# Kernel optimization log

Measured on AMD Instinct MI355X. Metric: run time of the kernel, lower is better.

Reference implementation:

```python
import jax, jax.numpy as jnp
import numpy as np

D_MODEL = 1024
NUM_HEADS = 16
D_K = D_MODEL // NUM_HEADS


def setup_inputs() -> dict:
    key = jax.random.key(0)
    ks = jax.random.split(key, 11)
    B, S = 2, 2048
    scale = 1.0 / np.sqrt(D_MODEL)
    inp = {
        "Q": jax.random.normal(ks[0], (B, S, D_MODEL), jnp.float32),
        "K": jax.random.normal(ks[1], (B, S, D_MODEL), jnp.float32),
        "V": jax.random.normal(ks[2], (B, S, D_MODEL), jnp.float32),
        # per-head projection weights stacked on head axis: [H, d_model, d_k]
        "Wq": jax.random.uniform(ks[3], (NUM_HEADS, D_MODEL, D_K), jnp.float32, -scale, scale),
        "bq": jax.random.uniform(ks[4], (NUM_HEADS, D_K), jnp.float32, -scale, scale),
        "Wk": jax.random.uniform(ks[5], (NUM_HEADS, D_MODEL, D_K), jnp.float32, -scale, scale),
        "bk": jax.random.uniform(ks[6], (NUM_HEADS, D_K), jnp.float32, -scale, scale),
        "Wv": jax.random.uniform(ks[7], (NUM_HEADS, D_MODEL, D_K), jnp.float32, -scale, scale),
        "bv": jax.random.uniform(ks[8], (NUM_HEADS, D_K), jnp.float32, -scale, scale),
        "Wo": jax.random.uniform(ks[9], (D_MODEL, D_MODEL), jnp.float32, -scale, scale),
        "bo": jax.random.uniform(ks[10], (D_MODEL,), jnp.float32, -scale, scale),
    }
    return inp


def reference(Q, K, V, Wq, bq, Wk, bk, Wv, bv, Wo, bo):
    # Batched equivalent of the per-head loop: project all heads at once.
    q = jnp.einsum("bsd,hdk->bhsk", Q, Wq) + bq[None, :, None, :]
    k = jnp.einsum("bsd,hdk->bhsk", K, Wk) + bk[None, :, None, :]
    v = jnp.einsum("bsd,hdk->bhsk", V, Wv) + bv[None, :, None, :]
    scores = jnp.einsum("bhqk,bhmk->bhqm", q, k) / jnp.sqrt(jnp.float32(D_K))
    weights = jax.nn.softmax(scores, axis=-1)
    attn = jnp.einsum("bhqm,bhmk->bhqk", weights, v)  # [B,H,S,d_k]
    B, H, S, Dk = attn.shape
    concat = attn.transpose(0, 2, 1, 3).reshape(B, S, H * Dk)  # head-order concat
    return concat @ Wo.T + bo
```

## Files before the change

### kernel.cpp

```cpp
#include <hip/hip_runtime.h>
#include <math.h>

#define BATCH 2
#define SLEN 2048
#define DM 1024
#define NH 16
#define DK 64
#define STILES (SLEN / 64)

typedef __attribute__((ext_vector_type(8))) __bf16 bf16x8;
typedef __attribute__((ext_vector_type(4))) float f32x4;

__device__ __forceinline__ unsigned short f2bf(float x) {
  unsigned u = __builtin_bit_cast(unsigned, x);
  unsigned r = (u + 0x7fffu + ((u >> 16) & 1u)) >> 16;
  return (unsigned short)r;
}
__device__ __forceinline__ float bf2f(unsigned short b) {
  unsigned u = ((unsigned)b) << 16;
  return __builtin_bit_cast(float, u);
}
__device__ __forceinline__ void splitbf(float x, unsigned short& h,
                                        unsigned short& l) {
  unsigned u = __builtin_bit_cast(unsigned, x);
  h = (unsigned short)(u >> 16);
  float hf = __builtin_bit_cast(float, u & 0xffff0000u);
  l = (unsigned short)(__builtin_bit_cast(unsigned, x - hf) >> 16);
}

__device__ __forceinline__ void gld16(const unsigned short* g,
                                      unsigned short* l) {
  __builtin_amdgcn_global_load_lds(
      (const __attribute__((address_space(1))) void*)g,
      (__attribute__((address_space(3))) void*)l, 16, 0, 0);
}

__global__ __launch_bounds__(256)
void convert_w(const float* __restrict__ Wq, const float* __restrict__ Wk,
               const float* __restrict__ Wv, unsigned short* __restrict__ Wqt,
               unsigned short* __restrict__ Wkt,
               unsigned short* __restrict__ Wvt) {
  const int kb = blockIdx.x, h = blockIdx.y, z = blockIdx.z;
  const float* W = (z == 0 ? Wq : z == 1 ? Wk : Wv) +
                   ((size_t)h * DM + kb * 64) * DK;
  unsigned short* D = (z == 0 ? Wqt : z == 1 ? Wkt : Wvt);

  __shared__ float T[64][65];
  const int tid = threadIdx.x;
  {
    int r = tid >> 2, c0 = (tid & 3) * 16;
#pragma unroll
    for (int i = 0; i < 4; ++i) {
      float4 f = *(const float4*)(W + (size_t)r * DK + c0 + i * 4);
      T[r][c0 + i * 4 + 0] = f.x;
      T[r][c0 + i * 4 + 1] = f.y;
      T[r][c0 + i * 4 + 2] = f.z;
      T[r][c0 + i * 4 + 3] = f.w;
    }
  }
  __syncthreads();
  int j = tid >> 2, p = tid & 3;
  int n = h * 64 + j;
  int kloc = p * 16;
  unsigned short hi[16], lo[16];
#pragma unroll
  for (int i = 0; i < 16; ++i) splitbf(T[kloc + i][j], hi[i], lo[i]);
  int kglob = kb * 64 + kloc;
  int blk = kglob >> 5;
  int c0 = (kglob & 31) >> 3;
  int key = n & 7;
  unsigned short* rowp = D + (size_t)n * 2048 + blk * 64;
  uint4 u0, u1;
  u0.x = (unsigned)hi[0] | ((unsigned)hi[1] << 16);
  u0.y = (unsigned)hi[2] | ((unsigned)hi[3] << 16);
  u0.z = (unsigned)hi[4] | ((unsigned)hi[5] << 16);
  u0.w = (unsigned)hi[6] | ((unsigned)hi[7] << 16);
  u1.x = (unsigned)hi[8] | ((unsigned)hi[9] << 16);
  u1.y = (unsigned)hi[10] | ((unsigned)hi[11] << 16);
  u1.z = (unsigned)hi[12] | ((unsigned)hi[13] << 16);
  u1.w = (unsigned)hi[14] | ((unsigned)hi[15] << 16);
  *(uint4*)(rowp + ((c0 ^ key)) * 8) = u0;
  *(uint4*)(rowp + (((c0 + 1) ^ key)) * 8) = u1;
  u0.x = (unsigned)lo[0] | ((unsigned)lo[1] << 16);
  u0.y = (unsigned)lo[2] | ((unsigned)lo[3] << 16);
  u0.z = (unsigned)lo[4] | ((unsigned)lo[5] << 16);
  u0.w = (unsigned)lo[6] | ((unsigned)lo[7] << 16);
  u1.x = (unsigned)lo[8] | ((unsigned)lo[9] << 16);
  u1.y = (unsigned)lo[10] | ((unsigned)lo[11] << 16);
  u1.z = (unsigned)lo[12] | ((unsigned)lo[13] << 16);
  u1.w = (unsigned)lo[14] | ((unsigned)lo[15] << 16);
  *(uint4*)(rowp + (((c0 + 4) ^ key)) * 8) = u0;
  *(uint4*)(rowp + (((c0 + 5) ^ key)) * 8) = u1;
}

__global__ __launch_bounds__(256)
void convert_wo(const float* __restrict__ Wo, unsigned short* __restrict__ Wot) {
  const int n = blockIdx.x;
  const int t = threadIdx.x;
  const int k0 = t * 4;
  float4 f = *(const float4*)(Wo + (size_t)n * DM + k0);
  ushort4 h4, l4;
  splitbf(f.x, h4.x, l4.x);
  splitbf(f.y, h4.y, l4.y);
  splitbf(f.z, h4.z, l4.z);
  splitbf(f.w, h4.w, l4.w);
  int blk = k0 >> 5, ch = (k0 & 31) >> 3, off = k0 & 7, key = n & 7;
  unsigned short* rowp = Wot + (size_t)n * 2048 + blk * 64;
  *(ushort4*)(rowp + ((ch ^ key)) * 8 + off) = h4;
  *(ushort4*)(rowp + (((ch + 4) ^ key)) * 8 + off) = l4;
}

__global__ __launch_bounds__(256)
void proj_gemm(const float* __restrict__ Qin, const float* __restrict__ Kin,
               const float* __restrict__ Vin,
               const unsigned short* __restrict__ Wqt,
               const unsigned short* __restrict__ Wkt,
               const unsigned short* __restrict__ Wvt,
               const float* __restrict__ bq, const float* __restrict__ bk,
               const float* __restrict__ bv, unsigned short* __restrict__ q_all,
               unsigned short* __restrict__ k_all,
               unsigned short* __restrict__ vt) {
  const int ntile = blockIdx.x, mt = blockIdx.y, z = blockIdx.z;
  const float* A = (z == 0 ? Qin : z == 1 ? Kin : Vin);
  const unsigned short* B = (z == 0 ? Wqt : z == 1 ? Wkt : Wvt);
  const float* bias = (z == 0 ? bq : z == 1 ? bk : bv);

  __shared__ alignas(16) unsigned short As[2][128 * 64];
  __shared__ alignas(16) unsigned short Bs[2][128 * 64];

  const int tid = threadIdx.x;
  const int lane = tid & 63, w = tid >> 6;
  const int l15 = lane & 15, quad = lane >> 4;
  const int wm = (w & 1) * 64, wn = (w >> 1) * 64;
  const int kx = l15 & 7;

  const float* Ap = A + (size_t)(mt * 128) * DM;
  const unsigned short* Bp = B + (size_t)(ntile * 128) * 2048;

  float4 areg[4];
#pragma unroll
  for (int it = 0; it < 4; ++it) {
    int c = tid + it * 256;
    int r = c >> 3, seg = c & 7;
    areg[it] = *(const float4*)(Ap + (size_t)r * DM + seg * 4);
  }
#pragma unroll
  for (int it = 0; it < 4; ++it) {
    int s = tid + it * 256;
    int r = s >> 3, seg = s & 7;
    gld16(Bp + (size_t)r * 2048 + seg * 8, &Bs[0][s * 8]);
  }

  f32x4 acc[4][4];
#pragma unroll
  for (int i = 0; i < 4; ++i)
#pragma unroll
    for (int j = 0; j < 4; ++j) acc[i][j] = (f32x4){0.f, 0.f, 0.f, 0.f};

  int cur = 0;
  for (int kk = 0; kk < 32; ++kk) {
#pragma unroll
    for (int it = 0; it < 4; ++it) {
      int c = tid + it * 256;
      int r = c >> 3, seg = c & 7;
      int key = r & 7, ch = seg >> 1, off = (seg & 1) * 4;
      ushort4 h4, l4;
      splitbf(areg[it].x, h4.x, l4.x);
      splitbf(areg[it].y, h4.y, l4.y);
      splitbf(areg[it].z, h4.z, l4.z);
      splitbf(areg[it].w, h4.w, l4.w);
      *(ushort4*)&As[cur][r * 64 + ((ch ^ key)) * 8 + off] = h4;
      *(ushort4*)&As[cur][r * 64 + (((ch + 4) ^ key)) * 8 + off] = l4;
    }
    __syncthreads();

    if (kk + 1 < 32) {
      int k0n = (kk + 1) * 32;
#pragma unroll
      for (int it = 0; it < 4; ++it) {
        int c = tid + it * 256;
        int r = c >> 3, seg = c & 7;
        areg[it] = *(const float4*)(Ap + (size_t)r * DM + k0n + seg * 4);
      }
#pragma unroll
      for (int it = 0; it < 4; ++it) {
        int s = tid + it * 256;
        int r = s >> 3, seg = s & 7;
        gld16(Bp + (size_t)r * 2048 + (k0n >> 5) * 64 + seg * 8,
              &Bs[cur ^ 1][s * 8]);
      }
    }

    bf16x8 ah[4], al[4];
#pragma unroll
    for (int i = 0; i < 4; ++i) {
      const unsigned short* p = &As[cur][(wm + i * 16 + l15) * 64];
      ah[i] = *(const bf16x8*)(p + ((quad ^ kx)) * 8);
      al[i] = *(const bf16x8*)(p + (((quad + 4) ^ kx)) * 8);
    }
#pragma unroll
    for (int j = 0; j < 4; ++j) {
      const unsigned short* p = &Bs[cur][(wn + j * 16 + l15) * 64];
      bf16x8 bh = *(const bf16x8*)(p + ((quad ^ kx)) * 8);
      bf16x8 bl = *(const bf16x8*)(p + (((quad + 4) ^ kx)) * 8);
#pragma unroll
      for (int i = 0; i < 4; ++i) {
        acc[i][j] = __builtin_amdgcn_mfma_f32_16x16x32_bf16(ah[i], bh, acc[i][j], 0, 0, 0);
        acc[i][j] = __builtin_amdgcn_mfma_f32_16x16x32_bf16(al[i], bh, acc[i][j], 0, 0, 0);
        acc[i][j] = __builtin_amdgcn_mfma_f32_16x16x32_bf16(ah[i], bl, acc[i][j], 0, 0, 0);
      }
    }
    cur ^= 1;
  }

  if (z <= 1) {
    unsigned short* dst = (z == 0 ? q_all : k_all);
#pragma unroll
    for (int i = 0; i < 4; ++i)
#pragma unroll
      for (int j = 0; j < 4; ++j) {
        int n = ntile * 128 + wn + j * 16 + l15;
        int hh_ = n >> 6, d = n & 63;
        int chi = (d >> 5) * 8 + ((d & 31) >> 3);
        float bn = bias[n];
#pragma unroll
        for (int r = 0; r < 4; ++r) {
          int m = mt * 128 + wm + i * 16 + quad * 4 + r;
          int key = m & 15;
          size_t rb = (size_t)m * 2048 + hh_ * 128;
          unsigned short hv, lv;
          splitbf(acc[i][j][r] + bn, hv, lv);
          dst[rb + ((chi ^ key)) * 8 + (d & 7)] = hv;
          dst[rb + (((chi + 4) ^ key)) * 8 + (d & 7)] = lv;
        }
      }
  } else {
#pragma unroll
    for (int i = 0; i < 4; ++i)
#pragma unroll
      for (int j = 0; j < 4; ++j) {
        int n = ntile * 128 + wn + j * 16 + l15;
        int h = n >> 6, d = n & 63;
        float bn = bias[n];
        int m0 = mt * 128 + wm + i * 16 + quad * 4;
        int b = m0 >> 11, s0_ = m0 & 2047;
        int kt = s0_ >> 6, sl = s0_ & 63;
        int ch = sl >> 3, off = sl & 7, key = d & 15;
        ushort4 h4, l4;
        splitbf(acc[i][j][0] + bn, h4.x, l4.x);
        splitbf(acc[i][j][1] + bn, h4.y, l4.y);
        splitbf(acc[i][j][2] + bn, h4.z, l4.z);
        splitbf(acc[i][j][3] + bn, h4.w, l4.w);
        size_t base =
            (size_t)(b * NH + h) * 262144 + (size_t)d * 4096 + kt * 128;
        *(ushort4*)(vt + base + ((ch ^ key)) * 8 + off) = h4;
        *(ushort4*)(vt + base + (((ch + 8) ^ key)) * 8 + off) = l4;
      }
  }
}

__global__ __launch_bounds__(256)
void out_gemm(const unsigned short* __restrict__ a_all,
              const unsigned short* __restrict__ Wot,
              const float* __restrict__ bo, float* __restrict__ out) {
  const int ntile = blockIdx.x, mt = blockIdx.y;

  __shared__ alignas(16) unsigned short As[2][64 * 64];
  __shared__ alignas(16) unsigned short Bs[2][128 * 64];

  const int tid = threadIdx.x;
  const int lane = tid & 63, w = tid >> 6;
  const int l15 = lane & 15, quad = lane >> 4;
  const int wn = w * 32;
  const int kx = l15 & 7;

  const unsigned short* Ap = a_all + (size_t)(mt * 64) * 2048;
  const unsigned short* Bp = Wot + (size_t)(ntile * 128) * 2048;

#pragma unroll
  for (int it = 0; it < 2; ++it) {
    int s = tid + it * 256;
    int r = s >> 3, seg = s & 7;
    gld16(Ap + (size_t)r * 2048 + seg * 8, &As[0][s * 8]);
  }
#pragma unroll
  for (int it = 0; it < 4; ++it) {
    int s = tid + it * 256;
    int r = s >> 3, seg = s & 7;
    gld16(Bp + (size_t)r * 2048 + seg * 8, &Bs[0][s * 8]);
  }

  f32x4 acc[4][2];
#pragma unroll
  for (int i = 0; i < 4; ++i)
#pragma unroll
    for (int j = 0; j < 2; ++j) acc[i][j] = (f32x4){0.f, 0.f, 0.f, 0.f};

  int cur = 0;
  for (int kk = 0; kk < 32; ++kk) {
    __syncthreads();

    if (kk + 1 < 32) {
      int blk = ((kk + 1)) * 64;
#pragma unroll
      for (int it = 0; it < 2; ++it) {
        int s = tid + it * 256;
        int r = s >> 3, seg = s & 7;
        gld16(Ap + (size_t)r * 2048 + blk + seg * 8, &As[cur ^ 1][s * 8]);
      }
#pragma unroll
      for (int it = 0; it < 4; ++it) {
        int s = tid + it * 256;
        int r = s >> 3, seg = s & 7;
        gld16(Bp + (size_t)r * 2048 + blk + seg * 8, &Bs[cur ^ 1][s * 8]);
      }
    }

    bf16x8 ah[4], al[4];
#pragma unroll
    for (int i = 0; i < 4; ++i) {
      const unsigned short* p = &As[cur][(i * 16 + l15) * 64];
      ah[i] = *(const bf16x8*)(p + ((quad ^ kx)) * 8);
      al[i] = *(const bf16x8*)(p + (((quad + 4) ^ kx)) * 8);
    }
#pragma unroll
    for (int j = 0; j < 2; ++j) {
      const unsigned short* p = &Bs[cur][(wn + j * 16 + l15) * 64];
      bf16x8 bh = *(const bf16x8*)(p + ((quad ^ kx)) * 8);
      bf16x8 bl = *(const bf16x8*)(p + (((quad + 4) ^ kx)) * 8);
#pragma unroll
      for (int i = 0; i < 4; ++i) {
        acc[i][j] = __builtin_amdgcn_mfma_f32_16x16x32_bf16(ah[i], bh, acc[i][j], 0, 0, 0);
        acc[i][j] = __builtin_amdgcn_mfma_f32_16x16x32_bf16(al[i], bh, acc[i][j], 0, 0, 0);
        acc[i][j] = __builtin_amdgcn_mfma_f32_16x16x32_bf16(ah[i], bl, acc[i][j], 0, 0, 0);
      }
    }
    cur ^= 1;
  }

#pragma unroll
  for (int i = 0; i < 4; ++i)
#pragma unroll
    for (int j = 0; j < 2; ++j) {
      int n = ntile * 128 + wn + j * 16 + l15;
      float bn = bo[n];
#pragma unroll
      for (int r = 0; r < 4; ++r) {
        int m = mt * 64 + i * 16 + quad * 4 + r;
        out[(size_t)m * DM + n] = acc[i][j][r] + bn;
      }
    }
}

__global__ __launch_bounds__(256)
void attn_kernel(const unsigned short* __restrict__ q_all,
                 const unsigned short* __restrict__ k_all,
                 const unsigned short* __restrict__ vt,
                 unsigned short* __restrict__ a_all) {
  const int qt = blockIdx.x, h = blockIdx.y, b = blockIdx.z;
  const unsigned short* vp = vt + (size_t)(b * NH + h) * 262144;

  __shared__ alignas(16) unsigned short Ks[64 * 128];
  __shared__ alignas(16) unsigned short Vs[64 * 128];
  __shared__ alignas(16) unsigned short Ps[128 * 64];

  const int tid = threadIdx.x;
  const int lane = tid & 63;
  const int w = tid >> 6;
  const int l15 = lane & 15;
  const int quad = lane >> 4;

  bf16x8 qf[2][2][2];
#pragma unroll
  for (int rt = 0; rt < 2; ++rt) {
    const unsigned short* qrow =
        q_all + (size_t)(b * SLEN + qt * 128 + w * 32 + rt * 16 + l15) * 2048 +
        h * 128;
#pragma unroll
    for (int kb = 0; kb < 2; ++kb) {
      qf[rt][kb][0] = *(const bf16x8*)(qrow + ((kb * 8 + quad) ^ l15) * 8);
      qf[rt][kb][1] = *(const bf16x8*)(qrow + ((kb * 8 + quad + 4) ^ l15) * 8);
    }
  }

  f32x4 o[2][4];
  float lpart[2][4];
#pragma unroll
  for (int rt = 0; rt < 2; ++rt)
#pragma unroll
    for (int nt = 0; nt < 4; ++nt) {
      o[rt][nt] = (f32x4){0.f, 0.f, 0.f, 0.f};
      lpart[rt][nt] = 0.f;
    }

  for (int kt = 0; kt < STILES; ++kt) {
    const unsigned short* ksrc =
        k_all + (size_t)(b * SLEN + kt * 64) * 2048 + h * 128;
#pragma unroll
    for (int it = 0; it < 4; ++it) {
      int ss = it * 256 + tid;
      int r = ss >> 4, p = ss & 15;
      gld16(ksrc + (size_t)r * 2048 + p * 8, &Ks[ss * 8]);
    }
#pragma unroll
    for (int it = 0; it < 4; ++it) {
      int ss = it * 256 + tid;
      int d = ss >> 4, p = ss & 15;
      gld16(vp + (size_t)d * 4096 + kt * 128 + p * 8, &Vs[ss * 8]);
    }
    __syncthreads();

    f32x4 sc[2][4];
#pragma unroll
    for (int rt = 0; rt < 2; ++rt)
#pragma unroll
      for (int ct = 0; ct < 4; ++ct) sc[rt][ct] = (f32x4){0.f, 0.f, 0.f, 0.f};
#pragma unroll
    for (int ct = 0; ct < 4; ++ct) {
      const unsigned short* kbase = &Ks[(ct * 16 + l15) * 128];
#pragma unroll
      for (int kb = 0; kb < 2; ++kb) {
        bf16x8 kh = *(const bf16x8*)(kbase + ((kb * 8 + quad) ^ l15) * 8);
        bf16x8 kl = *(const bf16x8*)(kbase + ((kb * 8 + quad + 4) ^ l15) * 8);
#pragma unroll
        for (int rt = 0; rt < 2; ++rt) {
          sc[rt][ct] = __builtin_amdgcn_mfma_f32_16x16x32_bf16(qf[rt][kb][0], kh, sc[rt][ct], 0, 0, 0);
          sc[rt][ct] = __builtin_amdgcn_mfma_f32_16x16x32_bf16(qf[rt][kb][0], kl, sc[rt][ct], 0, 0, 0);
          sc[rt][ct] = __builtin_amdgcn_mfma_f32_16x16x32_bf16(qf[rt][kb][1], kh, sc[rt][ct], 0, 0, 0);
        }
      }
    }

#pragma unroll
    for (int rt = 0; rt < 2; ++rt)
#pragma unroll
      for (int ct = 0; ct < 4; ++ct)
#pragma unroll
        for (int r = 0; r < 4; ++r) {
          float e = __expf(sc[rt][ct][r] * 0.125f);
          lpart[rt][r] += e;
          int prow = w * 32 + rt * 16 + quad * 4 + r;
          int pkey = (prow >> 1) & 7;
          Ps[prow * 64 + (((ct * 2 + (l15 >> 3)) ^ pkey)) * 8 + (l15 & 7)] =
              f2bf(e);
        }
    __syncthreads();

    int rk = (l15 >> 1) & 7;
#pragma unroll
    for (int kb = 0; kb < 2; ++kb) {
      bf16x8 pf[2];
#pragma unroll
      for (int rt = 0; rt < 2; ++rt)
        pf[rt] = *(const bf16x8*)(&Ps[(w * 32 + rt * 16 + l15) * 64 +
                                      (((kb * 4 + quad) ^ rk)) * 8]);
#pragma unroll
      for (int nt = 0; nt < 4; ++nt) {
        const unsigned short* vb = &Vs[(nt * 16 + l15) * 128];
        bf16x8 vh = *(const bf16x8*)(vb + (((kb * 4 + quad) ^ l15)) * 8);
        bf16x8 vl = *(const bf16x8*)(vb + (((kb * 4 + quad + 8) ^ l15)) * 8);
#pragma unroll
        for (int rt = 0; rt < 2; ++rt) {
          o[rt][nt] = __builtin_amdgcn_mfma_f32_16x16x32_bf16(pf[rt], vh, o[rt][nt], 0, 0, 0);
          o[rt][nt] = __builtin_amdgcn_mfma_f32_16x16x32_bf16(pf[rt], vl, o[rt][nt], 0, 0, 0);
        }
      }
    }
    __syncthreads();
  }

#pragma unroll
  for (int rt = 0; rt < 2; ++rt) {
    float inv[4];
#pragma unroll
    for (int r = 0; r < 4; ++r) {
      float lv = lpart[rt][r];
#pragma unroll
      for (int m = 1; m < 16; m <<= 1) lv += __shfl_xor(lv, m, 64);
      inv[r] = 1.f / lv;
    }
#pragma unroll
    for (int nt = 0; nt < 4; ++nt) {
      int c = h * 64 + nt * 16 + l15;
      int Bb = c >> 5;
      int d32 = c & 31;
      int ch = d32 >> 3, off = d32 & 7;
#pragma unroll
      for (int r = 0; r < 4; ++r) {
        float val = o[rt][nt][r] * inv[r];
        int srow = qt * 128 + w * 32 + rt * 16 + quad * 4 + r;
        int key = srow & 7;
        size_t g = (size_t)(b * SLEN + srow) * 2048 + Bb * 64;
        unsigned short hv, lv2;
        splitbf(val, hv, lv2);
        a_all[g + ((ch ^ key)) * 8 + off] = hv;
        a_all[g + (((ch + 4) ^ key)) * 8 + off] = lv2;
      }
    }
  }
}

extern "C" void kernel_launch(void* const* d_in, const int* in_sizes, int n_in,
                              void* d_out, int out_size, void* d_ws,
                              size_t ws_size, hipStream_t stream) {
  (void)in_sizes; (void)n_in; (void)out_size; (void)ws_size;
  const float* Q = (const float*)d_in[0];
  const float* K = (const float*)d_in[1];
  const float* V = (const float*)d_in[2];
  const float* Wq = (const float*)d_in[3];
  const float* bq = (const float*)d_in[4];
  const float* Wk = (const float*)d_in[5];
  const float* bk = (const float*)d_in[6];
  const float* Wv = (const float*)d_in[7];
  const float* bv = (const float*)d_in[8];
  const float* Wo = (const float*)d_in[9];
  const float* bo = (const float*)d_in[10];
  float* out = (float*)d_out;

  unsigned short* us = (unsigned short*)d_ws;
  const size_t M8 = 8u * 1024 * 1024;
  unsigned short* q_all = us;
  unsigned short* k_all = us + M8;
  unsigned short* vt = us + 2 * M8;
  unsigned short* a_all = us + 3 * M8;
  unsigned short* Wqt = a_all;
  unsigned short* Wkt = a_all + 2 * 1024 * 1024;
  unsigned short* Wvt = a_all + 4 * 1024 * 1024;
  unsigned short* Wot = q_all;

  convert_w<<<dim3(16, 16, 3), 256, 0, stream>>>(Wq, Wk, Wv, Wqt, Wkt, Wvt);
  proj_gemm<<<dim3(8, 32, 3), 256, 0, stream>>>(Q, K, V, Wqt, Wkt, Wvt, bq,
                                                bk, bv, q_all, k_all, vt);
  attn_kernel<<<dim3(SLEN / 128, NH, BATCH), 256, 0, stream>>>(q_all, k_all,
                                                               vt, a_all);
  convert_wo<<<dim3(1024), 256, 0, stream>>>(Wo, Wot);
  out_gemm<<<dim3(8, 64), 256, 0, stream>>>(a_all, Wot, bo, out);
}
```

Measured before the change: 371.1 us.

## Pre-split activations to bf16 hi/lo and double-buffer K/V tiles in attention

```diff
diff --git a/kernel.cpp b/kernel.cpp
--- a/kernel.cpp
+++ b/kernel.cpp
@@ -15,10 +15,6 @@
   unsigned u = __builtin_bit_cast(unsigned, x);
   unsigned r = (u + 0x7fffu + ((u >> 16) & 1u)) >> 16;
   return (unsigned short)r;
-}
-__device__ __forceinline__ float bf2f(unsigned short b) {
-  unsigned u = ((unsigned)b) << 16;
-  return __builtin_bit_cast(float, u);
 }
 __device__ __forceinline__ void splitbf(float x, unsigned short& h,
                                         unsigned short& l) {
@@ -94,6 +90,26 @@
 }
 
 __global__ __launch_bounds__(256)
+void convert_x(const float* __restrict__ Q, const float* __restrict__ K,
+               const float* __restrict__ V, unsigned short* __restrict__ Xp) {
+  const int m = blockIdx.x, z = blockIdx.y;
+  const float* src = (z == 0 ? Q : z == 1 ? K : V) + (size_t)m * DM;
+  unsigned short* dst =
+      Xp + (size_t)z * (8u * 1024 * 1024) + (size_t)m * 2048;
+  const int k0 = threadIdx.x * 4;
+  float4 f = *(const float4*)(src + k0);
+  ushort4 h4, l4;
+  splitbf(f.x, h4.x, l4.x);
+  splitbf(f.y, h4.y, l4.y);
+  splitbf(f.z, h4.z, l4.z);
+  splitbf(f.w, h4.w, l4.w);
+  int blk = k0 >> 5, ch = (k0 & 31) >> 3, off = k0 & 7, key = m & 7;
+  unsigned short* rowp = dst + blk * 64;
+  *(ushort4*)(rowp + ((ch ^ key)) * 8 + off) = h4;
+  *(ushort4*)(rowp + (((ch + 4) ^ key)) * 8 + off) = l4;
+}
+
+__global__ __launch_bounds__(256)
 void convert_wo(const float* __restrict__ Wo, unsigned short* __restrict__ Wot) {
   const int n = blockIdx.x;
   const int t = threadIdx.x;
@@ -111,8 +127,7 @@
 }
 
 __global__ __launch_bounds__(256)
-void proj_gemm(const float* __restrict__ Qin, const float* __restrict__ Kin,
-               const float* __restrict__ Vin,
+void proj_gemm(const unsigned short* __restrict__ Xp,
                const unsigned short* __restrict__ Wqt,
                const unsigned short* __restrict__ Wkt,
                const unsigned short* __restrict__ Wvt,
@@ -121,7 +136,6 @@
                unsigned short* __restrict__ k_all,
                unsigned short* __restrict__ vt) {
   const int ntile = blockIdx.x, mt = blockIdx.y, z = blockIdx.z;
-  const float* A = (z == 0 ? Qin : z == 1 ? Kin : Vin);
   const unsigned short* B = (z == 0 ? Wqt : z == 1 ? Wkt : Wvt);
   const float* bias = (z == 0 ? bq : z == 1 ? bk : bv);
 
@@ -134,20 +148,15 @@
   const int wm = (w & 1) * 64, wn = (w >> 1) * 64;
   const int kx = l15 & 7;
 
-  const float* Ap = A + (size_t)(mt * 128) * DM;
+  const unsigned short* Ap =
+      Xp + (size_t)z * (8u * 1024 * 1024) + (size_t)(mt * 128) * 2048;
   const unsigned short* Bp = B + (size_t)(ntile * 128) * 2048;
 
-  float4 areg[4];
-#pragma unroll
-  for (int it = 0; it < 4; ++it) {
-    int c = tid + it * 256;
-    int r = c >> 3, seg = c & 7;
-    areg[it] = *(const float4*)(Ap + (size_t)r * DM + seg * 4);
-  }
 #pragma unroll
   for (int it = 0; it < 4; ++it) {
     int s = tid + it * 256;
     int r = s >> 3, seg = s & 7;
+    gld16(Ap + (size_t)r * 2048 + seg * 8, &As[0][s * 8]);
     gld16(Bp + (size_t)r * 2048 + seg * 8, &Bs[0][s * 8]);
   }
 
@@ -159,35 +168,16 @@
 
   int cur = 0;
   for (int kk = 0; kk < 32; ++kk) {
-#pragma unroll
-    for (int it = 0; it < 4; ++it) {
-      int c = tid + it * 256;
-      int r = c >> 3, seg = c & 7;
-      int key = r & 7, ch = seg >> 1, off = (seg & 1) * 4;
-      ushort4 h4, l4;
-      splitbf(areg[it].x, h4.x, l4.x);
-      splitbf(areg[it].y, h4.y, l4.y);
-      splitbf(areg[it].z, h4.z, l4.z);
-      splitbf(areg[it].w, h4.w, l4.w);
-      *(ushort4*)&As[cur][r * 64 + ((ch ^ key)) * 8 + off] = h4;
-      *(ushort4*)&As[cur][r * 64 + (((ch + 4) ^ key)) * 8 + off] = l4;
-    }
     __syncthreads();
 
     if (kk + 1 < 32) {
-      int k0n = (kk + 1) * 32;
-#pragma unroll
-      for (int it = 0; it < 4; ++it) {
-        int c = tid + it * 256;
-        int r = c >> 3, seg = c & 7;
-        areg[it] = *(const float4*)(Ap + (size_t)r * DM + k0n + seg * 4);
-      }
+      int blk = (kk + 1) * 64;
 #pragma unroll
       for (int it = 0; it < 4; ++it) {
         int s = tid + it * 256;
         int r = s >> 3, seg = s & 7;
-        gld16(Bp + (size_t)r * 2048 + (k0n >> 5) * 64 + seg * 8,
-              &Bs[cur ^ 1][s * 8]);
+        gld16(Ap + (size_t)r * 2048 + blk + seg * 8, &As[cur ^ 1][s * 8]);
+        gld16(Bp + (size_t)r * 2048 + blk + seg * 8, &Bs[cur ^ 1][s * 8]);
       }
     }
 
@@ -301,7 +291,7 @@
     __syncthreads();
 
     if (kk + 1 < 32) {
-      int blk = ((kk + 1)) * 64;
+      int blk = (kk + 1) * 64;
 #pragma unroll
       for (int it = 0; it < 2; ++it) {
         int s = tid + it * 256;
@@ -360,8 +350,8 @@
   const int qt = blockIdx.x, h = blockIdx.y, b = blockIdx.z;
   const unsigned short* vp = vt + (size_t)(b * NH + h) * 262144;
 
-  __shared__ alignas(16) unsigned short Ks[64 * 128];
-  __shared__ alignas(16) unsigned short Vs[64 * 128];
+  __shared__ alignas(16) unsigned short Ks[2][64 * 128];
+  __shared__ alignas(16) unsigned short Vs[2][64 * 128];
   __shared__ alignas(16) unsigned short Ps[128 * 64];
 
   const int tid = threadIdx.x;
@@ -383,6 +373,22 @@
     }
   }
 
+  {
+    const unsigned short* ksrc = k_all + (size_t)(b * SLEN) * 2048 + h * 128;
+#pragma unroll
+    for (int it = 0; it < 4; ++it) {
+      int ss = it * 256 + tid;
+      int r = ss >> 4, p = ss & 15;
+      gld16(ksrc + (size_t)r * 2048 + p * 8, &Ks[0][ss * 8]);
+    }
+#pragma unroll
+    for (int it = 0; it < 4; ++it) {
+      int ss = it * 256 + tid;
+      int d = ss >> 4, p = ss & 15;
+      gld16(vp + (size_t)d * 4096 + p * 8, &Vs[0][ss * 8]);
+    }
+  }
+
   f32x4 o[2][4];
   float lpart[2][4];
 #pragma unroll
@@ -393,23 +399,28 @@
       lpart[rt][nt] = 0.f;
     }
 
+  int cur = 0;
   for (int kt = 0; kt < STILES; ++kt) {
-    const unsigned short* ksrc =
-        k_all + (size_t)(b * SLEN + kt * 64) * 2048 + h * 128;
-#pragma unroll
-    for (int it = 0; it < 4; ++it) {
-      int ss = it * 256 + tid;
-      int r = ss >> 4, p = ss & 15;
-      gld16(ksrc + (size_t)r * 2048 + p * 8, &Ks[ss * 8]);
-    }
-#pragma unroll
-    for (int it = 0; it < 4; ++it) {
-      int ss = it * 256 + tid;
-      int d = ss >> 4, p = ss & 15;
-      gld16(vp + (size_t)d * 4096 + kt * 128 + p * 8, &Vs[ss * 8]);
-    }
     __syncthreads();
 
+    if (kt + 1 < STILES) {
+      const unsigned short* ksrc =
+          k_all + (size_t)(b * SLEN + (kt + 1) * 64) * 2048 + h * 128;
+#pragma unroll
+      for (int it = 0; it < 4; ++it) {
+        int ss = it * 256 + tid;
+        int r = ss >> 4, p = ss & 15;
+        gld16(ksrc + (size_t)r * 2048 + p * 8, &Ks[cur ^ 1][ss * 8]);
+      }
+#pragma unroll
+      for (int it = 0; it < 4; ++it) {
+        int ss = it * 256 + tid;
+        int d = ss >> 4, p = ss & 15;
+        gld16(vp + (size_t)d * 4096 + (kt + 1) * 128 + p * 8,
+              &Vs[cur ^ 1][ss * 8]);
+      }
+    }
+
     f32x4 sc[2][4];
 #pragma unroll
     for (int rt = 0; rt < 2; ++rt)
@@ -417,7 +428,7 @@
       for (int ct = 0; ct < 4; ++ct) sc[rt][ct] = (f32x4){0.f, 0.f, 0.f, 0.f};
 #pragma unroll
     for (int ct = 0; ct < 4; ++ct) {
-      const unsigned short* kbase = &Ks[(ct * 16 + l15) * 128];
+      const unsigned short* kbase = &Ks[cur][(ct * 16 + l15) * 128];
 #pragma unroll
       for (int kb = 0; kb < 2; ++kb) {
         bf16x8 kh = *(const bf16x8*)(kbase + ((kb * 8 + quad) ^ l15) * 8);
@@ -456,7 +467,7 @@
                                       (((kb * 4 + quad) ^ rk)) * 8]);
 #pragma unroll
       for (int nt = 0; nt < 4; ++nt) {
-        const unsigned short* vb = &Vs[(nt * 16 + l15) * 128];
+        const unsigned short* vb = &Vs[cur][(nt * 16 + l15) * 128];
         bf16x8 vh = *(const bf16x8*)(vb + (((kb * 4 + quad) ^ l15)) * 8);
         bf16x8 vl = *(const bf16x8*)(vb + (((kb * 4 + quad + 8) ^ l15)) * 8);
 #pragma unroll
@@ -467,6 +478,7 @@
       }
     }
     __syncthreads();
+    cur ^= 1;
   }
 
 #pragma unroll
@@ -526,11 +538,13 @@
   unsigned short* Wqt = a_all;
   unsigned short* Wkt = a_all + 2 * 1024 * 1024;
   unsigned short* Wvt = a_all + 4 * 1024 * 1024;
+  unsigned short* Xp = us + 4 * M8;
   unsigned short* Wot = q_all;
 
   convert_w<<<dim3(16, 16, 3), 256, 0, stream>>>(Wq, Wk, Wv, Wqt, Wkt, Wvt);
-  proj_gemm<<<dim3(8, 32, 3), 256, 0, stream>>>(Q, K, V, Wqt, Wkt, Wvt, bq,
-                                                bk, bv, q_all, k_all, vt);
+  convert_x<<<dim3(4096, 3), 256, 0, stream>>>(Q, K, V, Xp);
+  proj_gemm<<<dim3(8, 32, 3), 256, 0, stream>>>(Xp, Wqt, Wkt, Wvt, bq, bk, bv,
+                                                q_all, k_all, vt);
   attn_kernel<<<dim3(SLEN / 128, NH, BATCH), 256, 0, stream>>>(q_all, k_all,
                                                                vt, a_all);
   convert_wo<<<dim3(1024), 256, 0, stream>>>(Wo, Wot);
```

Result: no change. 367.8 us (-0.9%).
